# Performance work log

Hardware: AMD Instinct MI355X
Metric: run time of the kernel (lower is better)

The kernel has to match this reference:

```python
import jax, jax.numpy as jnp
import numpy as np

B, T, D, K = 16, 4096, 512, 256
ALPHA_MIN = 1e-6


def setup_inputs() -> dict:
    key = jax.random.key(0)
    ks = jax.random.split(key, 5)
    x = jax.random.normal(ks[0], (B, T, D), dtype=jnp.float32)
    # s_imag ~ U(-pi, pi) as in reset_parameters
    s_imag = jax.random.uniform(ks[1], (K,), minval=-np.pi, maxval=np.pi, dtype=jnp.float32)
    # s_real_raw = softplus^{-1}(target_alpha - alpha_min), target_alpha ~ U(0.01, 0.2)
    target_alpha = jax.random.uniform(ks[2], (K,), minval=0.01, maxval=0.2, dtype=jnp.float32)
    y = jnp.clip(target_alpha - ALPHA_MIN, 1e-8, None)
    s_real_raw = jnp.log(jnp.expm1(y))
    # projection weight/bias (spectral norm applied inside reference)
    W = jax.random.normal(ks[3], (K, D), dtype=jnp.float32) / np.sqrt(D)
    b = jnp.zeros((K,), dtype=jnp.float32)
    tau_raw = jnp.zeros((), dtype=jnp.float32)
    return {"x": x, "s_real_raw": s_real_raw, "s_imag": s_imag,
            "tau_raw": tau_raw, "W": W, "b": b}


def _spectral_normalize(W):
    # one power iteration from a fixed random u (mirrors torch spectral_norm buffer,
    # n_power_iterations=1, eps=1e-7); u,v are stop-gradiented like torch buffers.
    eps = 1e-7
    u0 = jax.random.normal(jax.random.key(42), (W.shape[0],), dtype=W.dtype)
    u0 = u0 / jnp.maximum(jnp.linalg.norm(u0), eps)
    v = W.T @ u0
    v = v / jnp.maximum(jnp.linalg.norm(v), eps)
    u = W @ v
    u = u / jnp.maximum(jnp.linalg.norm(u), eps)
    u = jax.lax.stop_gradient(u)
    v = jax.lax.stop_gradient(v)
    sigma = u @ (W @ v)
    return W / sigma


def reference(x, s_real_raw, s_imag, tau_raw, W, b):
    Bx, Tx, Dx = x.shape
    k = s_imag.shape[0]
    tau = jax.nn.softplus(tau_raw) + 1e-3
    alpha0 = (jax.nn.softplus(s_real_raw) + ALPHA_MIN) * tau  # [k]
    omega0 = s_imag * tau                                     # [k]
    # dt is None path: uniform normalized time step
    dt = jnp.asarray(1.0 / max(Tx - 1, 1), dtype=x.dtype)
    rho = jnp.exp(-alpha0 * dt)   # [k], time-invariant since dt is constant
    ct = jnp.cos(omega0 * dt)     # [k]
    st = jnp.sin(omega0 * dt)     # [k]
    # spectral-normalized linear drive u_t = W_sn x_t + b  -> [B,T,k]
    u = jnp.einsum('btd,kd->btk', x, _spectral_normalize(W)) + b

    def step(carry, u_t):
        c, s = carry  # each [B,k]
        c_new = rho * (c * ct - s * st) + u_t
        s_new = rho * (c * st + s * ct)
        return (c_new, s_new), (c_new, s_new)

    z0 = (jnp.zeros((Bx, k), x.dtype), jnp.zeros((Bx, k), x.dtype))
    _, (C, S) = jax.lax.scan(step, z0, jnp.swapaxes(u, 0, 1))  # [T,B,k] each
    C = jnp.swapaxes(C, 0, 1)
    S = jnp.swapaxes(S, 0, 1)
    return jnp.concatenate([C, S], axis=2)  # [B,T,2k]
```

## Files before the change

### kernel.cpp

```cpp
#include <hip/hip_runtime.h>

#define Bsz 16
#define Tsz 4096
#define Dsz 512
#define Ksz 256
#define Msz (Bsz * Tsz)
#define CHUNK 64
#define NCH (Tsz / CHUNK)

typedef __attribute__((ext_vector_type(8))) short short8;
typedef __attribute__((ext_vector_type(4))) float f32x4;

__device__ __forceinline__ unsigned int rotl32(unsigned int x, int d) {
  return (x << d) | (x >> (32 - d));
}

__device__ void threefry_pair(unsigned int c0, unsigned int c1,
                              unsigned int& o0, unsigned int& o1) {
  const unsigned int k0 = 0u, k1 = 42u;
  const unsigned int k2 = k0 ^ k1 ^ 0x1BD11BDAu;
  unsigned int x0 = c0 + k0;
  unsigned int x1 = c1 + k1;
#define TF_ROUND(r) { x0 += x1; x1 = rotl32(x1, (r)); x1 ^= x0; }
  TF_ROUND(13) TF_ROUND(15) TF_ROUND(26) TF_ROUND(6)
  x0 += k1; x1 += k2 + 1u;
  TF_ROUND(17) TF_ROUND(29) TF_ROUND(16) TF_ROUND(24)
  x0 += k2; x1 += k0 + 2u;
  TF_ROUND(13) TF_ROUND(15) TF_ROUND(26) TF_ROUND(6)
  x0 += k0; x1 += k1 + 3u;
  TF_ROUND(17) TF_ROUND(29) TF_ROUND(16) TF_ROUND(24)
  x0 += k1; x1 += k2 + 4u;
  TF_ROUND(13) TF_ROUND(15) TF_ROUND(26) TF_ROUND(6)
  x0 += k2; x1 += k0 + 5u;
#undef TF_ROUND
  o0 = x0; o1 = x1;
}

__device__ float erfinv32(float x) {
  float w = -log1pf(-x * x);
  float p;
  if (w < 5.f) {
    w -= 2.5f;
    p = 2.81022636e-08f;
    p = fmaf(p, w, 3.43273939e-07f);
    p = fmaf(p, w, -3.5233877e-06f);
    p = fmaf(p, w, -4.39150654e-06f);
    p = fmaf(p, w, 0.00021858087f);
    p = fmaf(p, w, -0.00125372503f);
    p = fmaf(p, w, -0.00417768164f);
    p = fmaf(p, w, 0.246640727f);
    p = fmaf(p, w, 1.50140941f);
  } else {
    w = sqrtf(w) - 3.f;
    p = -0.000200214257f;
    p = fmaf(p, w, 0.000100950558f);
    p = fmaf(p, w, 0.00134934322f);
    p = fmaf(p, w, -0.00367342844f);
    p = fmaf(p, w, 0.00573950773f);
    p = fmaf(p, w, -0.0076224613f);
    p = fmaf(p, w, 0.00943887047f);
    p = fmaf(p, w, 1.00167406f);
    p = fmaf(p, w, 2.83297682f);
  }
  return p * x;
}

__device__ float bits_to_normal(unsigned int bits) {
  unsigned int fb = (bits >> 9) | 0x3f800000u;
  float f = __uint_as_float(fb) - 1.0f;
  const float lo = -0.99999994f;
  float u = f * 2.0f + lo;
  u = fmaxf(lo, u);
  return 1.41421356f * erfinv32(u);
}

__device__ float block_sum_512(float v, float* s_red) {
  #pragma unroll
  for (int o = 32; o > 0; o >>= 1) v += __shfl_down(v, o);
  const int lane = threadIdx.x & 63, wid = threadIdx.x >> 6;
  if (lane == 0) s_red[wid] = v;
  __syncthreads();
  float r = 0.f;
  #pragma unroll
  for (int i = 0; i < 8; ++i) r += s_red[i];
  __syncthreads();
  return r;
}

__device__ __forceinline__ unsigned int bf16rne(float f) {
  unsigned int u = __float_as_uint(f);
  return (u + 0x7FFFu + ((u >> 16) & 1u)) >> 16;
}

__global__ __launch_bounds__(512) void prep1_kernel(
    const float* __restrict__ W, float* __restrict__ partial_v) {
  __shared__ float s_u0[Ksz];
  __shared__ float s_red[8];
  const int tid = threadIdx.x;
  if (tid < 128) {
    unsigned int y0, y1;
    threefry_pair((unsigned int)tid, (unsigned int)(tid + 128), y0, y1);
    s_u0[tid] = bits_to_normal(y0);
    s_u0[tid + 128] = bits_to_normal(y1);
  }
  __syncthreads();
  float val = (tid < Ksz) ? s_u0[tid] * s_u0[tid] : 0.f;
  float ss = block_sum_512(val, s_red);
  float inv = 1.f / fmaxf(sqrtf(ss), 1e-7f);

  const int k0 = blockIdx.x * 16;
  float acc = 0.f;
  #pragma unroll
  for (int kk = 0; kk < 16; ++kk)
    acc = fmaf(W[(size_t)(k0 + kk) * Dsz + tid], s_u0[k0 + kk], acc);
  partial_v[blockIdx.x * Dsz + tid] = acc * inv;
}

__global__ __launch_bounds__(512) void prep2_kernel(
    const float* __restrict__ W, const float* __restrict__ partial_v,
    float* __restrict__ wv) {
  __shared__ float s_v[Dsz];
  __shared__ float s_red[8];
  __shared__ float s_p[8];
  const int tid = threadIdx.x;
  float acc = 0.f;
  #pragma unroll
  for (int b = 0; b < 16; ++b) acc += partial_v[b * Dsz + tid];
  float ssv = block_sum_512(acc * acc, s_red);
  float invv = 1.f / fmaxf(sqrtf(ssv), 1e-7f);
  s_v[tid] = acc * invv;
  __syncthreads();

  const int k = blockIdx.x * 4 + (tid >> 7);
  const int sub = tid & 127;
  const float* wr = W + (size_t)k * Dsz;
  float p = 0.f;
  #pragma unroll
  for (int j = sub; j < Dsz; j += 128) p = fmaf(wr[j], s_v[j], p);
  #pragma unroll
  for (int o = 32; o > 0; o >>= 1) p += __shfl_down(p, o);
  const int lane = tid & 63, wid = tid >> 6;
  if (lane == 0) s_p[wid] = p;
  __syncthreads();
  if (tid < 4) wv[blockIdx.x * 4 + tid] = s_p[2 * tid] + s_p[2 * tid + 1];
}

__global__ __launch_bounds__(256) void prep3_kernel(
    const float* __restrict__ s_real_raw, const float* __restrict__ s_imag,
    const float* __restrict__ tau_raw, const float* __restrict__ wv,
    float* __restrict__ consts) {
  __shared__ float s_p[4];
  const int tid = threadIdx.x;
  float v = wv[tid];
  float v2 = v * v;
  #pragma unroll
  for (int o = 32; o > 0; o >>= 1) v2 += __shfl_down(v2, o);
  const int lane = tid & 63, wid = tid >> 6;
  if (lane == 0) s_p[wid] = v2;
  __syncthreads();
  float sswv = s_p[0] + s_p[1] + s_p[2] + s_p[3];
  float sigma = sswv / fmaxf(sqrtf(sswv), 1e-7f);
  if (tid == 0) consts[10 * Ksz] = 1.f / sigma;

  float tr = tau_raw[0];
  float tau = fmaxf(tr, 0.f) + log1pf(expf(-fabsf(tr))) + 1e-3f;
  float srr = s_real_raw[tid];
  float sp = fmaxf(srr, 0.f) + log1pf(expf(-fabsf(srr)));
  float alpha0 = (sp + 1e-6f) * tau;
  float omega0 = s_imag[tid] * tau;
  const float dt = 1.f / 4095.f;
  float ad = alpha0 * dt, an = omega0 * dt;
  consts[tid]            = expf(-ad) * cosf(an);
  consts[Ksz + tid]      = expf(-ad) * sinf(an);
  consts[2 * Ksz + tid]  = expf(-ad * 64.f) * cosf(an * 64.f);
  consts[3 * Ksz + tid]  = expf(-ad * 64.f) * sinf(an * 64.f);
  consts[4 * Ksz + tid]  = expf(-ad * 4.f) * cosf(an * 4.f);
  consts[5 * Ksz + tid]  = expf(-ad * 4.f) * sinf(an * 4.f);
  consts[6 * Ksz + tid]  = expf(-ad * 8.f) * cosf(an * 8.f);
  consts[7 * Ksz + tid]  = expf(-ad * 8.f) * sinf(an * 8.f);
  consts[8 * Ksz + tid]  = expf(-ad * 16.f) * cosf(an * 16.f);
  consts[9 * Ksz + tid]  = expf(-ad * 16.f) * sinf(an * 16.f);
}

__global__ __launch_bounds__(64) void wpack_kernel(
    const float* __restrict__ W, const float* __restrict__ consts,
    unsigned int* __restrict__ WfH, unsigned int* __restrict__ WfL) {
  const int kb = blockIdx.x >> 4;
  const int nb = blockIdx.x & 15;
  const int lane = threadIdx.x;
  const int lr = lane & 15, lg = lane >> 4;
  const float inv_sigma = consts[10 * Ksz];
  const float* src = W + (size_t)(nb * 16 + lr) * Dsz + kb * 32 + lg * 8;
  float v[8];
  *(float4*)&v[0] = *(const float4*)src;
  *(float4*)&v[4] = *(const float4*)(src + 4);
  unsigned int hh[4], ll[4];
  #pragma unroll
  for (int i = 0; i < 4; ++i) {
    float v0 = v[2 * i] * inv_sigma, v1 = v[2 * i + 1] * inv_sigma;
    unsigned int u0 = __float_as_uint(v0);
    unsigned int u1 = __float_as_uint(v1);
    hh[i] = (u0 >> 16) | (u1 & 0xFFFF0000u);
    float r0 = v0 - __uint_as_float(u0 & 0xFFFF0000u);
    float r1 = v1 - __uint_as_float(u1 & 0xFFFF0000u);
    ll[i] = bf16rne(r0) | (bf16rne(r1) << 16);
  }
  const size_t off = (size_t)blockIdx.x * 256 + lane * 4;
  *(int4*)(WfH + off) = *(int4*)hh;
  *(int4*)(WfL + off) = *(int4*)ll;
}

__global__ __launch_bounds__(256, 2) void gemm_mfma(
    const float* __restrict__ X, const unsigned int* __restrict__ WfH,
    const unsigned int* __restrict__ WfL, const float* __restrict__ bias,
    const float* __restrict__ consts, float* __restrict__ U,
    float* __restrict__ carry) {
  __shared__ unsigned int ldsA[2][2048];

  const int tid = threadIdx.x;
  const size_t m0 = (size_t)blockIdx.x * 64;

  const int sr = tid >> 2;
  const int sc = (tid & 3) * 8;
  const float* gx = X + (m0 + sr) * Dsz + sc;
  const int swz = (sr & 7) << 4;
  const int aoff_h = sr * 128 + ((sc * 2) ^ swz);
  const int aoff_l = sr * 128 + ((64 + sc * 2) ^ swz);

  const int lane = tid & 63;
  const int wn = tid >> 6;
  const int lr = lane & 15;
  const int lg = lane >> 4;

  float xaA[8], xaB[8];
  #define LOAD_A(dst, kb) do {                             \
    const float* p = gx + (kb) * 32;                       \
    *(float4*)&dst[0] = *(const float4*)p;                 \
    *(float4*)&dst[4] = *(const float4*)(p + 4);           \
  } while (0)

  const char* const wfh = (const char*)WfH + (size_t)wn * 4096 + lane * 16;
  const char* const wfl = (const char*)WfL + (size_t)wn * 4096 + lane * 16;

  short8 bhA[4], blA[4], bhB[4], blB[4];
  #define LOAD_B(bh_, bl_, kb) do {                                          \
    const size_t tb = (size_t)(kb) * 16384;                                  \
    _Pragma("unroll")                                                        \
    for (int f = 0; f < 4; ++f) {                                            \
      bh_[f] = *(const short8*)(wfh + tb + (size_t)f * 1024);                \
      bl_[f] = *(const short8*)(wfl + tb + (size_t)f * 1024);                \
    }                                                                        \
  } while (0)

  LOAD_A(xaA, 0);
  LOAD_A(xaB, 1);
  LOAD_B(bhA, blA, 0);

  f32x4 acc[4][4];
  #pragma unroll
  for (int i = 0; i < 4; ++i)
    #pragma unroll
    for (int j = 0; j < 4; ++j) acc[i][j] = (f32x4)(0.f);

  #define BODY(kb, xa, bhC, blC, bhN, blN) do {                              \
    char* const Ab = (char*)ldsA[(kb) & 1];                                  \
    if ((kb) + 1 < 16) LOAD_B(bhN, blN, (kb) + 1);        \
                  \
    {                                                                        \
      unsigned int hh[4], llw[4];                                            \
      _Pragma("unroll")                                                      \
      for (int i = 0; i < 4; ++i) {                                          \
        float v0 = xa[2 * i], v1 = xa[2 * i + 1];                            \
        unsigned int u0 = __float_as_uint(v0);                               \
        unsigned int u1 = __float_as_uint(v1);                               \
        hh[i] = (u0 >> 16) | (u1 & 0xFFFF0000u);                             \
        float r0 = v0 - __uint_as_float(u0 & 0xFFFF0000u);                   \
        float r1 = v1 - __uint_as_float(u1 & 0xFFFF0000u);                   \
        llw[i] = bf16rne(r0) | (bf16rne(r1) << 16);                          \
      }                                                                      \
      *(int4*)(Ab + aoff_h) = *(int4*)hh;                                    \
      *(int4*)(Ab + aoff_l) = *(int4*)llw;                                   \
    }                                                                        \
    if ((kb) + 2 < 16) LOAD_A(xa, (kb) + 2);          \
    asm volatile("s_waitcnt lgkmcnt(0)" ::: "memory");                       \
    __builtin_amdgcn_s_barrier();                                            \
    __builtin_amdgcn_sched_barrier(0);                                       \
    short8 ah[4], al[4];                                                     \
    _Pragma("unroll")                                                        \
    for (int f = 0; f < 4; ++f) {                                            \
      const int r = f * 16 + lr;                                             \
      const int sz = (r & 7) << 4;                                           \
      ah[f] = *(const short8*)(Ab + r * 128 + ((lg * 16) ^ sz));             \
      al[f] = *(const short8*)(Ab + r * 128 + ((64 + lg * 16) ^ sz));        \
    }                                                                        \
    _Pragma("unroll")                                                        \
    for (int mf = 0; mf < 4; ++mf)                                           \
      _Pragma("unroll")                                                      \
      for (int nf = 0; nf < 4; ++nf)                                         \
        acc[mf][nf] = __builtin_amdgcn_mfma_f32_16x16x32_bf16(               \
            ah[mf], bhC[nf], acc[mf][nf], 0, 0, 0);                          \
    _Pragma("unroll")                                                        \
    for (int mf = 0; mf < 4; ++mf)                                           \
      _Pragma("unroll")                                                      \
      for (int nf = 0; nf < 4; ++nf)                                         \
        acc[mf][nf] = __builtin_amdgcn_mfma_f32_16x16x32_bf16(               \
            ah[mf], blC[nf], acc[mf][nf], 0, 0, 0);                          \
    _Pragma("unroll")                                                        \
    for (int mf = 0; mf < 4; ++mf)                                           \
      _Pragma("unroll")                                                      \
      for (int nf = 0; nf < 4; ++nf)                                         \
        acc[mf][nf] = __builtin_amdgcn_mfma_f32_16x16x32_bf16(               \
            al[mf], bhC[nf], acc[mf][nf], 0, 0, 0);                          \
  } while (0)

  for (int kb = 0; kb < 16; kb += 2) {
    BODY(kb,     xaA, bhA, blA, bhB, blB);
    BODY(kb + 1, xaB, bhB, blB, bhA, blA);
  }
  #undef BODY
  #undef LOAD_B
  #undef LOAD_A

  #pragma unroll
  for (int nf = 0; nf < 4; ++nf) {
    const int n = wn * 64 + nf * 16 + lr;
    const float bv = bias[n];
    const float ar_ = consts[n],           ai_ = consts[Ksz + n];
    const float p4r = consts[4 * Ksz + n], p4i = consts[5 * Ksz + n];
    const float p8r = consts[6 * Ksz + n], p8i = consts[7 * Ksz + n];
    const float p16r = consts[8 * Ksz + n], p16i = consts[9 * Ksz + n];
    const int e = 3 - lg;
    const float b1r = (e & 1) ? p4r : 1.f, b1i = (e & 1) ? p4i : 0.f;
    const float b2r = (e & 2) ? p8r : 1.f, b2i = (e & 2) ? p8i : 0.f;
    float wr = b1r * b2r - b1i * b2i;
    float wi = b1r * b2i + b1i * b2r;
    float Sr = 0.f, Si = 0.f;
    #pragma unroll
    for (int mf = 3; mf >= 0; --mf) {
      float vr = wr, vi = wi;
      #pragma unroll
      for (int j = 3; j >= 0; --j) {
        const float u = acc[mf][nf][j] + bv;
        U[(m0 + mf * 16 + lg * 4 + j) * Ksz + n] = u;
        Sr = fmaf(u, vr, Sr);
        Si = fmaf(u, vi, Si);
        if (j) {
          float t_ = vr * ar_ - vi * ai_;
          vi = vr * ai_ + vi * ar_;
          vr = t_;
        }
      }
      if (mf) {
        float t_ = wr * p16r - wi * p16i;
        wi = wr * p16i + wi * p16r;
        wr = t_;
      }
    }
    Sr += __shfl_xor(Sr, 16); Si += __shfl_xor(Si, 16);
    Sr += __shfl_xor(Sr, 32); Si += __shfl_xor(Si, 32);
    if (lg == 0)
      ((float2*)carry)[(size_t)blockIdx.x * Ksz + n] = make_float2(Sr, Si);
  }
}

__global__ __launch_bounds__(64) void scan_prefix(
    const float* __restrict__ consts, const float* __restrict__ carry,
    float* __restrict__ prefix) {
  const int k = blockIdx.y * 64 + threadIdx.x;
  const int b = blockIdx.x;
  const float Ar = consts[2 * Ksz + k], Ai = consts[3 * Ksz + k];
  const float2* cp = (const float2*)carry;
  float2* pp = (float2*)prefix;
  float c = 0.f, s = 0.f;
  for (int m = 0; m < NCH; ++m) {
    const size_t idx = (size_t)(b * NCH + m) * Ksz + k;
    pp[idx] = make_float2(c, s);
    float2 L = cp[idx];
    float cn = fmaf(Ar, c, fmaf(-Ai, s, L.x));
    float sn = fmaf(Ai, c, fmaf(Ar, s, L.y));
    c = cn; s = sn;
  }
}

__global__ __launch_bounds__(256) void scan_final(
    const float* __restrict__ U, const float* __restrict__ consts,
    const float* __restrict__ prefix, float* __restrict__ out) {
  const int k = threadIdx.x;
  const int bm = blockIdx.x;
  const float ar = consts[k], ai = consts[Ksz + k];
  float2 w = ((const float2*)prefix)[(size_t)bm * Ksz + k];
  float c = w.x, s = w.y;
  const float* up = U + (size_t)bm * (CHUNK * Ksz) + k;
  float* op = out + (size_t)bm * (CHUNK * 2 * Ksz);
  #pragma unroll 4
  for (int t = 0; t < CHUNK; ++t) {
    float u = up[(size_t)t * Ksz];
    float cn = fmaf(ar, c, fmaf(-ai, s, u));
    s = fmaf(ai, c, ar * s);
    c = cn;
    op[(size_t)t * 2 * Ksz + k] = c;
    op[(size_t)t * 2 * Ksz + Ksz + k] = s;
  }
}

extern "C" void kernel_launch(void* const* d_in, const int* in_sizes, int n_in,
                              void* d_out, int out_size, void* d_ws, size_t ws_size,
                              hipStream_t stream) {
  const float* x    = (const float*)d_in[0];
  const float* srr  = (const float*)d_in[1];
  const float* sim  = (const float*)d_in[2];
  const float* traw = (const float*)d_in[3];
  const float* W    = (const float*)d_in[4];
  const float* bias = (const float*)d_in[5];
  float* out = (float*)d_out;

  float* wsf    = (float*)d_ws;
  float* consts = wsf;
  float* U      = wsf + 4096;
  float* carry  = U + (size_t)Msz * Ksz;
  float* prefix = carry + (size_t)2 * Bsz * NCH * Ksz;
  unsigned int* WfH = (unsigned int*)(prefix + (size_t)2 * Bsz * NCH * Ksz);
  unsigned int* WfL = WfH + 65536;
  float* partial_v  = (float*)(WfL + 65536);
  float* wv         = partial_v + 16 * Dsz;

  prep1_kernel<<<16, 512, 0, stream>>>(W, partial_v);
  prep2_kernel<<<64, 512, 0, stream>>>(W, partial_v, wv);
  prep3_kernel<<<1, 256, 0, stream>>>(srr, sim, traw, wv, consts);
  wpack_kernel<<<256, 64, 0, stream>>>(W, consts, WfH, WfL);
  gemm_mfma<<<Msz / 64, 256, 0, stream>>>(x, WfH, WfL, bias, consts, U, carry);
  scan_prefix<<<dim3(Bsz, Ksz / 64), 64, 0, stream>>>(consts, carry, prefix);
  scan_final<<<Bsz * NCH, Ksz, 0, stream>>>(U, consts, prefix, out);
}
```

Baseline: 124.8 us.

## Software-pipeline LDS fragment reads ahead of MFMAs in the projection GEMM loop

Restructures the GEMM main loop so the LDS fragment reads for the next k-block are issued before the current block's 48 MFMAs. The bf16 hi/lo split of the A tile is now written to LDS after the MFMAs, and A global loads are prefetched two k-blocks further ahead. A prologue fills both LDS buffers before the loop starts. The aim is to hide LDS read latency behind matrix work and keep one barrier per k-block. The risk is that the B-fragment global loads for the next block are now issued later, just before the barrier, which may leave their latency exposed. Register pressure also rises from the extra fragment buffers.

```diff
diff --git a/kernel.cpp b/kernel.cpp
--- a/kernel.cpp
+++ b/kernel.cpp
@@ -252,72 +252,99 @@
     }                                                                        \
   } while (0)
 
-  LOAD_A(xaA, 0);
-  LOAD_A(xaB, 1);
-  LOAD_B(bhA, blA, 0);
-
-  f32x4 acc[4][4];
-  #pragma unroll
-  for (int i = 0; i < 4; ++i)
-    #pragma unroll
-    for (int j = 0; j < 4; ++j) acc[i][j] = (f32x4)(0.f);
-
-  #define BODY(kb, xa, bhC, blC, bhN, blN) do {                              \
-    char* const Ab = (char*)ldsA[(kb) & 1];                                  \
-    if ((kb) + 1 < 16) LOAD_B(bhN, blN, (kb) + 1);        \
-                  \
-    {                                                                        \
-      unsigned int hh[4], llw[4];                                            \
-      _Pragma("unroll")                                                      \
-      for (int i = 0; i < 4; ++i) {                                          \
-        float v0 = xa[2 * i], v1 = xa[2 * i + 1];                            \
-        unsigned int u0 = __float_as_uint(v0);                               \
-        unsigned int u1 = __float_as_uint(v1);                               \
-        hh[i] = (u0 >> 16) | (u1 & 0xFFFF0000u);                             \
-        float r0 = v0 - __uint_as_float(u0 & 0xFFFF0000u);                   \
-        float r1 = v1 - __uint_as_float(u1 & 0xFFFF0000u);                   \
-        llw[i] = bf16rne(r0) | (bf16rne(r1) << 16);                          \
-      }                                                                      \
-      *(int4*)(Ab + aoff_h) = *(int4*)hh;                                    \
-      *(int4*)(Ab + aoff_l) = *(int4*)llw;                                   \
+  #define CONVERT_STORE(xa, buf) do {                                        \
+    char* const Ab_ = (char*)ldsA[(buf)];                                    \
+    unsigned int hh[4], llw[4];                                              \
+    _Pragma("unroll")                                                        \
+    for (int i = 0; i < 4; ++i) {                                            \
+      float v0 = xa[2 * i], v1 = xa[2 * i + 1];                              \
+      unsigned int u0 = __float_as_uint(v0);                                 \
+      unsigned int u1 = __float_as_uint(v1);                                 \
+      hh[i] = (u0 >> 16) | (u1 & 0xFFFF0000u);                               \
+      float r0 = v0 - __uint_as_float(u0 & 0xFFFF0000u);                     \
+      float r1 = v1 - __uint_as_float(u1 & 0xFFFF0000u);                     \
+      llw[i] = bf16rne(r0) | (bf16rne(r1) << 16);                            \
     }                                                                        \
-    if ((kb) + 2 < 16) LOAD_A(xa, (kb) + 2);          \
-    asm volatile("s_waitcnt lgkmcnt(0)" ::: "memory");                       \
-    __builtin_amdgcn_s_barrier();                                            \
-    __builtin_amdgcn_sched_barrier(0);                                       \
-    short8 ah[4], al[4];                                                     \
+    *(int4*)(Ab_ + aoff_h) = *(int4*)hh;                                     \
+    *(int4*)(Ab_ + aoff_l) = *(int4*)llw;                                    \
+  } while (0)
+
+  #define DS_READ(ah_, al_, buf) do {                                        \
+    const char* const Ab_ = (const char*)ldsA[(buf)];                        \
     _Pragma("unroll")                                                        \
     for (int f = 0; f < 4; ++f) {                                            \
       const int r = f * 16 + lr;                                             \
       const int sz = (r & 7) << 4;                                           \
-      ah[f] = *(const short8*)(Ab + r * 128 + ((lg * 16) ^ sz));             \
-      al[f] = *(const short8*)(Ab + r * 128 + ((64 + lg * 16) ^ sz));        \
+      ah_[f] = *(const short8*)(Ab_ + r * 128 + ((lg * 16) ^ sz));           \
+      al_[f] = *(const short8*)(Ab_ + r * 128 + ((64 + lg * 16) ^ sz));      \
     }                                                                        \
+  } while (0)
+
+  #define MFMA48(ah_, al_, bh_, bl_) do {                                    \
     _Pragma("unroll")                                                        \
     for (int mf = 0; mf < 4; ++mf)                                           \
       _Pragma("unroll")                                                      \
       for (int nf = 0; nf < 4; ++nf)                                         \
         acc[mf][nf] = __builtin_amdgcn_mfma_f32_16x16x32_bf16(               \
-            ah[mf], bhC[nf], acc[mf][nf], 0, 0, 0);                          \
+            ah_[mf], bh_[nf], acc[mf][nf], 0, 0, 0);                         \
     _Pragma("unroll")                                                        \
     for (int mf = 0; mf < 4; ++mf)                                           \
       _Pragma("unroll")                                                      \
       for (int nf = 0; nf < 4; ++nf)                                         \
         acc[mf][nf] = __builtin_amdgcn_mfma_f32_16x16x32_bf16(               \
-            ah[mf], blC[nf], acc[mf][nf], 0, 0, 0);                          \
+            ah_[mf], bl_[nf], acc[mf][nf], 0, 0, 0);                         \
     _Pragma("unroll")                                                        \
     for (int mf = 0; mf < 4; ++mf)                                           \
       _Pragma("unroll")                                                      \
       for (int nf = 0; nf < 4; ++nf)                                         \
         acc[mf][nf] = __builtin_amdgcn_mfma_f32_16x16x32_bf16(               \
-            al[mf], bhC[nf], acc[mf][nf], 0, 0, 0);                          \
+            al_[mf], bh_[nf], acc[mf][nf], 0, 0, 0);                         \
+  } while (0)
+
+  #define SYNC() do {                                                        \
+    asm volatile("s_waitcnt lgkmcnt(0)" ::: "memory");                       \
+    __builtin_amdgcn_s_barrier();                                            \
+    __builtin_amdgcn_sched_barrier(0);                                       \
+  } while (0)
+
+  f32x4 acc[4][4];
+  #pragma unroll
+  for (int i = 0; i < 4; ++i)
+    #pragma unroll
+    for (int j = 0; j < 4; ++j) acc[i][j] = (f32x4)(0.f);
+
+  short8 ahA[4], alA[4], ahB[4], alB[4];
+
+  LOAD_A(xaA, 0);
+  LOAD_A(xaB, 1);
+  LOAD_B(bhA, blA, 0);
+  CONVERT_STORE(xaA, 0);
+  LOAD_A(xaA, 2);
+  SYNC();
+  DS_READ(ahA, alA, 0);
+  CONVERT_STORE(xaB, 1);
+  LOAD_A(xaB, 3);
+  SYNC();
+
+  #define BODY(kb, fragCh, fragCl, fragNh, fragNl, bCh, bCl, bNh, bNl, xa)   \
+  do {                                                                       \
+    if ((kb) + 1 < 16) DS_READ(fragNh, fragNl, ((kb) + 1) & 1);              \
+    MFMA48(fragCh, fragCl, bCh, bCl);                                        \
+    if ((kb) + 2 < 16) CONVERT_STORE(xa, (kb) & 1);            \
+    if ((kb) + 4 < 16) LOAD_A(xa, (kb) + 4);                                 \
+    if ((kb) + 1 < 16) LOAD_B(bNh, bNl, (kb) + 1);                           \
+    SYNC();                                                                  \
   } while (0)
 
   for (int kb = 0; kb < 16; kb += 2) {
-    BODY(kb,     xaA, bhA, blA, bhB, blB);
-    BODY(kb + 1, xaB, bhB, blB, bhA, blA);
+    BODY(kb,     ahA, alA, ahB, alB, bhA, blA, bhB, blB, xaA);
+    BODY(kb + 1, ahB, alB, ahA, alA, bhB, blB, bhA, blA, xaB);
   }
   #undef BODY
+  #undef SYNC
+  #undef MFMA48
+  #undef DS_READ
+  #undef CONVERT_STORE
   #undef LOAD_B
   #undef LOAD_A
 
```

New measurement: 127.2 us. Within noise of the previous version (+1.9%).

## Load A fragments directly from global into registers, removing LDS staging and barriers

Applied to the files above, without the earlier changes.

Each lane now loads its own A-fragment rows of X straight from global memory and converts them to bf16 hi/lo in registers, replacing the LDS write, the barrier and the LDS read. This removes LDS traffic and per-k-step block synchronisation. In exchange, all four waves redundantly load and convert the same 64xK tile of X, which quadruples global/L2 read traffic for A and the conversion ALU work, and register pressure rises because four sets of float fragments are double-buffered.

```diff
diff --git a/kernel.cpp b/kernel.cpp
--- a/kernel.cpp
+++ b/kernel.cpp
@@ -10,6 +10,7 @@
 
 typedef __attribute__((ext_vector_type(8))) short short8;
 typedef __attribute__((ext_vector_type(4))) float f32x4;
+typedef __attribute__((ext_vector_type(4))) unsigned int u32x4;
 
 __device__ __forceinline__ unsigned int rotl32(unsigned int x, int d) {
   return (x << d) | (x >> (32 - d));
@@ -215,34 +216,30 @@
     const unsigned int* __restrict__ WfL, const float* __restrict__ bias,
     const float* __restrict__ consts, float* __restrict__ U,
     float* __restrict__ carry) {
-  __shared__ unsigned int ldsA[2][2048];
-
   const int tid = threadIdx.x;
   const size_t m0 = (size_t)blockIdx.x * 64;
-
-  const int sr = tid >> 2;
-  const int sc = (tid & 3) * 8;
-  const float* gx = X + (m0 + sr) * Dsz + sc;
-  const int swz = (sr & 7) << 4;
-  const int aoff_h = sr * 128 + ((sc * 2) ^ swz);
-  const int aoff_l = sr * 128 + ((64 + sc * 2) ^ swz);
 
   const int lane = tid & 63;
   const int wn = tid >> 6;
   const int lr = lane & 15;
   const int lg = lane >> 4;
 
-  float xaA[8], xaB[8];
-  #define LOAD_A(dst, kb) do {                             \
-    const float* p = gx + (kb) * 32;                       \
-    *(float4*)&dst[0] = *(const float4*)p;                 \
-    *(float4*)&dst[4] = *(const float4*)(p + 4);           \
+  const float* gxa = X + (m0 + lr) * Dsz + lg * 8;
+
+  float xa0[4][8], xa1[4][8];
+  #define LOAD_A(dst, kb) do {                                               \
+    _Pragma("unroll")                                                        \
+    for (int mf = 0; mf < 4; ++mf) {                                         \
+      const float* p = gxa + mf * (16 * Dsz) + (kb) * 32;                    \
+      *(float4*)&dst[mf][0] = *(const float4*)p;                             \
+      *(float4*)&dst[mf][4] = *(const float4*)(p + 4);                       \
+    }                                                                        \
   } while (0)
 
   const char* const wfh = (const char*)WfH + (size_t)wn * 4096 + lane * 16;
   const char* const wfl = (const char*)WfL + (size_t)wn * 4096 + lane * 16;
 
-  short8 bhA[4], blA[4], bhB[4], blB[4];
+  short8 bh0[4], bl0[4], bh1[4], bl1[4];
   #define LOAD_B(bh_, bl_, kb) do {                                          \
     const size_t tb = (size_t)(kb) * 16384;                                  \
     _Pragma("unroll")                                                        \
@@ -252,25 +249,14 @@
     }                                                                        \
   } while (0)
 
-  LOAD_A(xaA, 0);
-  LOAD_A(xaB, 1);
-  LOAD_B(bhA, blA, 0);
-
-  f32x4 acc[4][4];
-  #pragma unroll
-  for (int i = 0; i < 4; ++i)
-    #pragma unroll
-    for (int j = 0; j < 4; ++j) acc[i][j] = (f32x4)(0.f);
-
-  #define BODY(kb, xa, bhC, blC, bhN, blN) do {                              \
-    char* const Ab = (char*)ldsA[(kb) & 1];                                  \
-    if ((kb) + 1 < 16) LOAD_B(bhN, blN, (kb) + 1);        \
-                  \
-    {                                                                        \
+  short8 ah[4], al[4];
+  #define CONVERT(xa) do {                                                   \
+    _Pragma("unroll")                                                        \
+    for (int mf = 0; mf < 4; ++mf) {                                         \
       unsigned int hh[4], llw[4];                                            \
       _Pragma("unroll")                                                      \
       for (int i = 0; i < 4; ++i) {                                          \
-        float v0 = xa[2 * i], v1 = xa[2 * i + 1];                            \
+        float v0 = xa[mf][2 * i], v1 = xa[mf][2 * i + 1];                    \
         unsigned int u0 = __float_as_uint(v0);                               \
         unsigned int u1 = __float_as_uint(v1);                               \
         hh[i] = (u0 >> 16) | (u1 & 0xFFFF0000u);                             \
@@ -278,46 +264,63 @@
         float r1 = v1 - __uint_as_float(u1 & 0xFFFF0000u);                   \
         llw[i] = bf16rne(r0) | (bf16rne(r1) << 16);                          \
       }                                                                      \
-      *(int4*)(Ab + aoff_h) = *(int4*)hh;                                    \
-      *(int4*)(Ab + aoff_l) = *(int4*)llw;                                   \
+      u32x4 th = {hh[0], hh[1], hh[2], hh[3]};                               \
+      u32x4 tl = {llw[0], llw[1], llw[2], llw[3]};                           \
+      ah[mf] = __builtin_bit_cast(short8, th);                               \
+      al[mf] = __builtin_bit_cast(short8, tl);                               \
     }                                                                        \
-    if ((kb) + 2 < 16) LOAD_A(xa, (kb) + 2);          \
-    asm volatile("s_waitcnt lgkmcnt(0)" ::: "memory");                       \
-    __builtin_amdgcn_s_barrier();                                            \
-    __builtin_amdgcn_sched_barrier(0);                                       \
-    short8 ah[4], al[4];                                                     \
-    _Pragma("unroll")                                                        \
-    for (int f = 0; f < 4; ++f) {                                            \
-      const int r = f * 16 + lr;                                             \
-      const int sz = (r & 7) << 4;                                           \
-      ah[f] = *(const short8*)(Ab + r * 128 + ((lg * 16) ^ sz));             \
-      al[f] = *(const short8*)(Ab + r * 128 + ((64 + lg * 16) ^ sz));        \
-    }                                                                        \
+  } while (0)
+
+  f32x4 acc[4][4];
+  #pragma unroll
+  for (int i = 0; i < 4; ++i)
+    #pragma unroll
+    for (int j = 0; j < 4; ++j) acc[i][j] = (f32x4)(0.f);
+
+  #define MFMA48(bh_, bl_) do {                                              \
     _Pragma("unroll")                                                        \
     for (int mf = 0; mf < 4; ++mf)                                           \
       _Pragma("unroll")                                                      \
       for (int nf = 0; nf < 4; ++nf)                                         \
         acc[mf][nf] = __builtin_amdgcn_mfma_f32_16x16x32_bf16(               \
-            ah[mf], bhC[nf], acc[mf][nf], 0, 0, 0);                          \
+            ah[mf], bh_[nf], acc[mf][nf], 0, 0, 0);                          \
     _Pragma("unroll")                                                        \
     for (int mf = 0; mf < 4; ++mf)                                           \
       _Pragma("unroll")                                                      \
       for (int nf = 0; nf < 4; ++nf)                                         \
         acc[mf][nf] = __builtin_amdgcn_mfma_f32_16x16x32_bf16(               \
-            ah[mf], blC[nf], acc[mf][nf], 0, 0, 0);                          \
+            ah[mf], bl_[nf], acc[mf][nf], 0, 0, 0);                          \
     _Pragma("unroll")                                                        \
     for (int mf = 0; mf < 4; ++mf)                                           \
       _Pragma("unroll")                                                      \
       for (int nf = 0; nf < 4; ++nf)                                         \
         acc[mf][nf] = __builtin_amdgcn_mfma_f32_16x16x32_bf16(               \
-            al[mf], bhC[nf], acc[mf][nf], 0, 0, 0);                          \
+            al[mf], bh_[nf], acc[mf][nf], 0, 0, 0);                          \
   } while (0)
 
-  for (int kb = 0; kb < 16; kb += 2) {
-    BODY(kb,     xaA, bhA, blA, bhB, blB);
-    BODY(kb + 1, xaB, bhB, blB, bhA, blA);
-  }
-  #undef BODY
+  LOAD_A(xa0, 0);
+  LOAD_A(xa1, 1);
+  LOAD_B(bh0, bl0, 0);
+
+  for (int kb = 0; kb < 14; kb += 2) {
+    CONVERT(xa0);
+    LOAD_A(xa0, kb + 2);
+    LOAD_B(bh1, bl1, kb + 1);
+    MFMA48(bh0, bl0);
+
+    CONVERT(xa1);
+    LOAD_A(xa1, kb + 3);
+    LOAD_B(bh0, bl0, kb + 2);
+    MFMA48(bh1, bl1);
+  }
+  CONVERT(xa0);
+  LOAD_B(bh1, bl1, 15);
+  MFMA48(bh0, bl0);
+  CONVERT(xa1);
+  MFMA48(bh1, bl1);
+
+  #undef MFMA48
+  #undef CONVERT
   #undef LOAD_B
   #undef LOAD_A
 
```

Measured after the change: 235.7 us. 1.89x slower.
